# Optimization experiments

Hardware: AMD Instinct MI355X
Metric: run time of the kernel (lower is better)

Reference implementation:

```python
import jax, jax.numpy as jnp
import numpy as np

N_NODES = 100000
N_EDGES = 1600000
N_QUERY = 200000
NODE_IN = 32
EDGE_IN = 8
H = 64
L = 3
LN_EPS = 1e-5
BN_EPS = 1e-5


def setup_inputs() -> dict:
    key = jax.random.key(0)
    ks = jax.random.split(key, 24)
    s = 1.0 / np.sqrt(H)
    inp = {
        "x": jax.random.normal(ks[0], (N_NODES, NODE_IN), jnp.float32),
        "edge_index": jax.random.randint(ks[1], (2, N_EDGES), 0, N_NODES, jnp.int32),
        "edge_attr": jax.random.normal(ks[2], (N_QUERY, EDGE_IN), jnp.float32),
        "query_edge_indices": jax.random.randint(ks[3], (2, N_QUERY), 0, N_NODES, jnp.int32),
        # node encoder
        "W_enc": jax.random.normal(ks[4], (NODE_IN, H), jnp.float32) * s,
        "b_enc": jnp.zeros((H,), jnp.float32),
        # SAGE layers: lin_l acts on concat(mean, max) -> [2H, H] with bias; lin_r on root [H, H] no bias
        "Wl": jax.random.normal(ks[5], (L, 2 * H, H), jnp.float32) * s,
        "bl": jnp.zeros((L, H), jnp.float32),
        "Wr": jax.random.normal(ks[6], (L, H, H), jnp.float32) * s,
        "ln_g": jnp.ones((L, H), jnp.float32),
        "ln_b": jnp.zeros((L, H), jnp.float32),
        # edge predictor MLP
        "W1": jax.random.normal(ks[7], (2 * H + EDGE_IN, 2 * H), jnp.float32) * s,
        "b1": jnp.zeros((2 * H,), jnp.float32),
        "bn_g": jnp.ones((2 * H,), jnp.float32),
        "bn_b": jnp.zeros((2 * H,), jnp.float32),
        "bn_mean": jnp.zeros((2 * H,), jnp.float32),
        "bn_var": jnp.ones((2 * H,), jnp.float32),
        "W2": jax.random.normal(ks[8], (2 * H, H), jnp.float32) * s,
        "b2": jnp.zeros((H,), jnp.float32),
        "W3": jax.random.normal(ks[9], (H, 1), jnp.float32) * s,
        "b3": jnp.zeros((1,), jnp.float32),
    }
    return inp


def _layer_norm(x, g, b):
    mu = jnp.mean(x, axis=-1, keepdims=True)
    var = jnp.var(x, axis=-1, keepdims=True)
    return (x - mu) * jax.lax.rsqrt(var + LN_EPS) * g + b


def _sage_conv(h, src, dst, Wl, bl, Wr):
    # gather neighbor messages, scatter-reduce to targets (mean and max), then linear combine
    m = h[src]  # [E, H]
    deg = jax.ops.segment_sum(jnp.ones((src.shape[0],), h.dtype), dst, num_segments=N_NODES)
    summed = jax.ops.segment_sum(m, dst, num_segments=N_NODES)
    mean = summed / jnp.maximum(deg, 1.0)[:, None]
    mx = jax.ops.segment_max(m, dst, num_segments=N_NODES)
    mx = jnp.where(deg[:, None] > 0, mx, 0.0)  # PyG fills isolated nodes with 0
    aggr = jnp.concatenate([mean, mx], axis=-1)  # [N, 2H]
    return aggr @ Wl + bl + h @ Wr


def reference(x, edge_index, edge_attr, query_edge_indices,
              W_enc, b_enc, Wl, bl, Wr, ln_g, ln_b,
              W1, b1, bn_g, bn_b, bn_mean, bn_var, W2, b2, W3, b3):
    src, dst = edge_index[0], edge_index[1]
    h = x @ W_enc + b_enc
    for i in range(L):
        h_res = h
        h = _sage_conv(h, src, dst, Wl[i], bl[i], Wr[i])
        h = _layer_norm(h, ln_g[i], ln_b[i])
        h = jax.nn.gelu(h, approximate=False)
        h = h + h_res  # dropout is identity in eval
    h_src = h[query_edge_indices[0]]
    h_tgt = h[query_edge_indices[1]]
    z = jnp.concatenate([h_src, h_tgt, edge_attr], axis=1)  # [Q, 2H+E]
    z = z @ W1 + b1
    z = (z - bn_mean) * jax.lax.rsqrt(bn_var + BN_EPS) * bn_g + bn_b  # BN eval mode
    z = jax.nn.gelu(z, approximate=False)
    z = jax.nn.gelu(z @ W2 + b2, approximate=False)
    return z @ W3 + b3
```

## Files before the change

### kernel.cpp

```cpp
#include <hip/hip_runtime.h>
#include <math.h>

#define N_NODES 100000
#define N_EDGES 1600000
#define N_QUERY 200000
#define NODE_IN 32
#define EDGE_IN 8
#define H 64
#define LAYERS 3
#define LN_EPS 1e-5f
#define BN_EPS 1e-5f
#define NBLK 391
#define NBUK 391
#define ACHUNK 4096
#define CAPB 6144

typedef __attribute__((ext_vector_type(8))) short short8b;
typedef __attribute__((ext_vector_type(4))) float f32x4;

__device__ __forceinline__ float gelu_f(float x){
    return 0.5f * x * (1.0f + erff(x * 0.70710678118654752440f));
}
__device__ __forceinline__ ushort f2bf(float x){
    unsigned u = __float_as_uint(x);
    unsigned r = (u + 0x7FFFu + ((u >> 16) & 1u)) >> 16;
    return (ushort)r;
}
__device__ __forceinline__ float bf2f(ushort x){
    return __uint_as_float(((unsigned)x) << 16);
}

__global__ __launch_bounds__(256) void k_zero_cnt(int* __restrict__ c){
    int i = blockIdx.x * 256 + threadIdx.x;
    if (i < N_NODES) c[i] = 0;
}
__global__ __launch_bounds__(256) void k_count(const int* __restrict__ ei, int* __restrict__ c){
    int i = blockIdx.x * 256 + threadIdx.x;
    if (i < N_EDGES) atomicAdd(&c[ei[N_EDGES + i]], 1);
}
__global__ __launch_bounds__(256) void k_scanA(const int* __restrict__ cnt, int* __restrict__ bsum){
    int i = blockIdx.x * 256 + threadIdx.x;
    int v = (i < N_NODES) ? cnt[i] : 0;
    #pragma unroll
    for (int off = 32; off; off >>= 1) v += __shfl_xor(v, off, 64);
    __shared__ int ws[4];
    if ((threadIdx.x & 63) == 0) ws[threadIdx.x >> 6] = v;
    __syncthreads();
    if (threadIdx.x == 0) bsum[blockIdx.x] = ws[0] + ws[1] + ws[2] + ws[3];
}
__global__ __launch_bounds__(512) void k_scanB(int* __restrict__ bsum){
    __shared__ int s[512];
    int t = threadIdx.x;
    int v = (t < NBLK) ? bsum[t] : 0;
    s[t] = v; __syncthreads();
    for (int off = 1; off < 512; off <<= 1){
        int u = (t >= off) ? s[t - off] : 0;
        __syncthreads();
        s[t] += u;
        __syncthreads();
    }
    if (t < NBLK) bsum[t] = s[t] - v;
}
__global__ __launch_bounds__(256) void k_scanC(const int* __restrict__ cnt, const int* __restrict__ bsum,
                                               int* __restrict__ rs){
    __shared__ int s[256];
    int t = threadIdx.x;
    int i = blockIdx.x * 256 + t;
    int v = (i < N_NODES) ? cnt[i] : 0;
    s[t] = v; __syncthreads();
    for (int off = 1; off < 256; off <<= 1){
        int u = (t >= off) ? s[t - off] : 0;
        __syncthreads();
        s[t] += u;
        __syncthreads();
    }
    int pref = bsum[blockIdx.x] + s[t] - v;
    if (i < N_NODES) rs[i] = pref;
    if (i == N_NODES - 1) rs[N_NODES] = pref + v;
}
__global__ __launch_bounds__(256) void k_init_bcur(const int* __restrict__ rs, int* __restrict__ bcur){
    int b = blockIdx.x * 256 + threadIdx.x;
    if (b < NBUK) bcur[b] = rs[b * 256];
}
__global__ __launch_bounds__(1024) void k_bucketA(const int* __restrict__ ei, int* __restrict__ bcur,
                                                  int* __restrict__ bucketed){
    __shared__ int hist[NBUK], pref[NBUK], curl[NBUK], gbase[NBUK];
    __shared__ int scan[512];
    __shared__ int stageP[ACHUNK];
    __shared__ ushort stageB[ACHUNK];
    int tid = threadIdx.x;
    int e0 = blockIdx.x * ACHUNK;
    int cnt = N_EDGES - e0;
    if (cnt > ACHUNK) cnt = ACHUNK;
    for (int b = tid; b < NBUK; b += 1024) hist[b] = 0;
    __syncthreads();
    int myd[4], mys[4];
    #pragma unroll
    for (int i = 0; i < 4; ++i){
        int idx = tid + i * 1024;
        if (idx < cnt){
            int e = e0 + idx;
            mys[i] = ei[e];
            myd[i] = ei[N_EDGES + e];
            atomicAdd(&hist[myd[i] >> 8], 1);
        } else myd[i] = -1;
    }
    __syncthreads();
    int v = (tid < NBUK) ? hist[tid] : 0;
    if (tid < 512) scan[tid] = v;
    __syncthreads();
    for (int off = 1; off < 512; off <<= 1){
        int u = 0;
        if (tid < 512 && tid >= off) u = scan[tid - off];
        __syncthreads();
        if (tid < 512) scan[tid] += u;
        __syncthreads();
    }
    if (tid < NBUK){
        int ex = scan[tid] - v;
        pref[tid] = ex;
        curl[tid] = ex;
        if (v > 0) gbase[tid] = atomicAdd(&bcur[tid], v);
    }
    __syncthreads();
    #pragma unroll
    for (int i = 0; i < 4; ++i){
        if (myd[i] >= 0){
            int b = myd[i] >> 8;
            int p = atomicAdd(&curl[b], 1);
            stageP[p] = (mys[i] << 8) | (myd[i] & 255);
            stageB[p] = (ushort)b;
        }
    }
    __syncthreads();
    for (int p = tid; p < cnt; p += 1024){
        int b = stageB[p];
        bucketed[gbase[b] + (p - pref[b])] = stageP[p];
    }
}
__global__ __launch_bounds__(1024) void k_fillB(const int* __restrict__ rs, int* __restrict__ csr){
    __shared__ int packed[CAPB];
    __shared__ int sorted[CAPB];
    __shared__ int hist[256], cur[256];
    __shared__ int scan[256];
    int tid = threadIdx.x;
    int node0 = blockIdx.x * 256;
    int node1 = node0 + 256; if (node1 > N_NODES) node1 = N_NODES;
    int r0 = rs[node0], r1 = rs[node1];
    int L = r1 - r0;
    if (tid < 256) hist[tid] = 0;
    __syncthreads();
    for (int i = tid; i < L; i += 1024){
        int pk = csr[r0 + i];
        packed[i] = pk;
        atomicAdd(&hist[pk & 255], 1);
    }
    __syncthreads();
    int v = (tid < 256) ? hist[tid] : 0;
    if (tid < 256) scan[tid] = v;
    __syncthreads();
    for (int off = 1; off < 256; off <<= 1){
        int u = 0;
        if (tid < 256 && tid >= off) u = scan[tid - off];
        __syncthreads();
        if (tid < 256) scan[tid] += u;
        __syncthreads();
    }
    if (tid < 256) cur[tid] = scan[tid] - v;
    __syncthreads();
    for (int i = tid; i < L; i += 1024){
        int pk = packed[i];
        int p = atomicAdd(&cur[pk & 255], 1);
        sorted[p] = pk >> 8;
    }
    __syncthreads();
    for (int i = tid; i < L; i += 1024) csr[r0 + i] = sorted[i];
}

__global__ __launch_bounds__(256) void k_enc(const float* __restrict__ x, const float* __restrict__ Wenc,
                                             const float* __restrict__ benc, float* __restrict__ h,
                                             ushort* __restrict__ hbf){
    __shared__ __align__(16) float sW[NODE_IN * H];
    __shared__ float sx[4][NODE_IN];
    int tid = threadIdx.x;
    int lane = tid & 63;
    int w = tid >> 6;
    int n = blockIdx.x * 4 + w;
    for (int i = tid; i < NODE_IN * H; i += 256) sW[i] = Wenc[i];
    if (n < N_NODES && lane < NODE_IN) sx[w][lane] = x[n * NODE_IN + lane];
    __syncthreads();
    if (n < N_NODES){
        float acc = benc[lane];
        #pragma unroll
        for (int k = 0; k < NODE_IN; ++k)
            acc = fmaf(sx[w][k], sW[k * H + lane], acc);
        h[n * H + lane] = acc;
        hbf[n * H + lane] = f2bf(acc);
    }
}

#define NT 32
__global__ __launch_bounds__(512, 4) void k_sage_mfma(const float* __restrict__ h,
    const ushort* __restrict__ hbf,
    const int* __restrict__ rs, const int* __restrict__ csr,
    const float* __restrict__ Wl, const float* __restrict__ bl, const float* __restrict__ Wr,
    const float* __restrict__ lng, const float* __restrict__ lnb,
    float* __restrict__ hout, ushort* __restrict__ hbfout)
{
    __shared__ __align__(16) ushort sAh[NT * 200];
    __shared__ __align__(16) ushort sAl[NT * 200];
    __shared__ __align__(16) ushort sW[64 * 200];
    __shared__ float2 sRed[8][16];
    const int tid = threadIdx.x;
    const int lane = tid & 63;
    const int w = tid >> 6;
    const int l15 = lane & 15;
    const int kb = lane >> 4;
    const int c4 = l15 * 4;
    const int n0 = blockIdx.x * NT;

    for (int i = tid; i < 128 * 64; i += 512){
        int k = i >> 6, f = i & 63;
        sW[f * 200 + k] = f2bf(Wl[i]);
    }
    for (int i = tid; i < 64 * 64; i += 512){
        int k = (i >> 6) + 128, f = i & 63;
        sW[f * 200 + k] = f2bf(Wr[i]);
    }

    for (int i = 0; i < 4; ++i){
        int nl = (w << 2) + i;
        int n = n0 + nl;
        float s0 = 0.f, s1 = 0.f, s2 = 0.f, s3 = 0.f;
        float m0 = -INFINITY, m1 = -INFINITY, m2 = -INFINITY, m3 = -INFINITY;
        int dg = 0;
        float4 hv4 = make_float4(0.f, 0.f, 0.f, 0.f);
        if (n < N_NODES){
            int start = rs[n], end = rs[n + 1];
            dg = end - start;
            hv4 = *(const float4*)(h + (size_t)n * H + c4);
            const int* cp = csr + start;
            int nfull = dg >> 2;
            #pragma unroll 4
            for (int j = 0; j < nfull; ++j){
                int s = cp[j * 4 + kb];
                const ushort4 u = *(const ushort4*)(hbf + ((size_t)s << 6) + c4);
                float v0 = bf2f(u.x), v1 = bf2f(u.y), v2 = bf2f(u.z), v3 = bf2f(u.w);
                s0 += v0; s1 += v1; s2 += v2; s3 += v3;
                m0 = fmaxf(m0, v0); m1 = fmaxf(m1, v1);
                m2 = fmaxf(m2, v2); m3 = fmaxf(m3, v3);
            }
            int rem = dg & 3;
            if (rem){
                int e = nfull * 4 + kb;
                int s = cp[(kb < rem) ? e : 0];
                const ushort4 u = *(const ushort4*)(hbf + ((size_t)s << 6) + c4);
                float v0 = bf2f(u.x), v1 = bf2f(u.y), v2 = bf2f(u.z), v3 = bf2f(u.w);
                bool val = kb < rem;
                s0 += val ? v0 : 0.f;  s1 += val ? v1 : 0.f;
                s2 += val ? v2 : 0.f;  s3 += val ? v3 : 0.f;
                m0 = fmaxf(m0, val ? v0 : -INFINITY);
                m1 = fmaxf(m1, val ? v1 : -INFINITY);
                m2 = fmaxf(m2, val ? v2 : -INFINITY);
                m3 = fmaxf(m3, val ? v3 : -INFINITY);
            }
        }
        #pragma unroll
        for (int off = 16; off < 64; off <<= 1){
            s0 += __shfl_xor(s0, off, 64); s1 += __shfl_xor(s1, off, 64);
            s2 += __shfl_xor(s2, off, 64); s3 += __shfl_xor(s3, off, 64);
            m0 = fmaxf(m0, __shfl_xor(m0, off, 64)); m1 = fmaxf(m1, __shfl_xor(m1, off, 64));
            m2 = fmaxf(m2, __shfl_xor(m2, off, 64)); m3 = fmaxf(m3, __shfl_xor(m3, off, 64));
        }
        float inv = (dg > 0) ? (1.f / (float)dg) : 0.f;
        float4 val;
        if (kb == 0)      val = make_float4(s0 * inv, s1 * inv, s2 * inv, s3 * inv);
        else if (kb == 1) val = (dg > 0) ? make_float4(m0, m1, m2, m3) : make_float4(0.f,0.f,0.f,0.f);
        else              val = hv4;
        if (kb < 3){
            ushort4 vh = { f2bf(val.x), f2bf(val.y), f2bf(val.z), f2bf(val.w) };
            ushort4 vl = { f2bf(val.x - bf2f(vh.x)), f2bf(val.y - bf2f(vh.y)),
                           f2bf(val.z - bf2f(vh.z)), f2bf(val.w - bf2f(vh.w)) };
            *(ushort4*)(sAh + nl * 200 + kb * 64 + c4) = vh;
            *(ushort4*)(sAl + nl * 200 + kb * 64 + c4) = vl;
        }
    }
    __syncthreads();

    f32x4 acc = (f32x4){0.f,0.f,0.f,0.f};
    const int rt = w & 1;
    const int c0 = (w >> 1) * 16;
    const int arow = (rt * 16 + l15) * 200 + kb * 8;
    const int brow = (c0 + l15) * 200 + kb * 8;
    #pragma unroll
    for (int kc = 0; kc < 6; ++kc){
        short8b ah = *(const short8b*)(sAh + arow + kc * 32);
        short8b al = *(const short8b*)(sAl + arow + kc * 32);
        short8b b  = *(const short8b*)(sW + brow + kc * 32);
        acc = __builtin_amdgcn_mfma_f32_16x16x32_bf16(ah, b, acc, 0, 0, 0);
        acc = __builtin_amdgcn_mfma_f32_16x16x32_bf16(al, b, acc, 0, 0, 0);
    }

    const int f = c0 + l15;
    float blf = bl[f], gf = lng[f], bfv = lnb[f];
    #pragma unroll
    for (int r = 0; r < 4; ++r) acc[r] += blf;
    f32x4 s1v, s2v;
    #pragma unroll
    for (int r = 0; r < 4; ++r){ s1v[r] = acc[r]; s2v[r] = acc[r] * acc[r]; }
    #pragma unroll
    for (int r = 0; r < 4; ++r){
        #pragma unroll
        for (int off = 1; off < 16; off <<= 1){
            s1v[r] += __shfl_xor(s1v[r], off, 64);
            s2v[r] += __shfl_xor(s2v[r], off, 64);
        }
    }
    if (l15 == 0){
        #pragma unroll
        for (int r = 0; r < 4; ++r) sRed[w][kb * 4 + r] = make_float2(s1v[r], s2v[r]);
    }
    __syncthreads();
    const int rowb = n0 + rt * 16 + kb * 4;
    #pragma unroll
    for (int r = 0; r < 4; ++r){
        int row = rowb + r;
        if (row < N_NODES){
            float2 p2 = sRed[w ^ 2][kb * 4 + r];
            float2 p4 = sRed[w ^ 4][kb * 4 + r];
            float2 p6 = sRed[w ^ 6][kb * 4 + r];
            float S1 = s1v[r] + p2.x + p4.x + p6.x;
            float S2 = s2v[r] + p2.y + p4.y + p6.y;
            float mu = S1 * (1.f / 64.f);
            float var = S2 * (1.f / 64.f) - mu * mu;
            float rsv = rsqrtf(var + LN_EPS);
            float y = (acc[r] - mu) * rsv * gf + bfv;
            float o = gelu_f(y) + h[row * H + f];
            hout[row * H + f] = o;
            hbfout[row * H + f] = f2bf(o);
        }
    }
}

#define QB 128
__global__ __launch_bounds__(512, 2) void k_mlp_mfma(const ushort* __restrict__ hbf,
    const int* __restrict__ qe, const float* __restrict__ ea,
    const float* __restrict__ W1, const float* __restrict__ b1,
    const float* __restrict__ bng, const float* __restrict__ bnb,
    const float* __restrict__ bnm, const float* __restrict__ bnv,
    const float* __restrict__ W2, const float* __restrict__ b2,
    const float* __restrict__ W3, const float* __restrict__ b3,
    float* __restrict__ out)
{
    __shared__ __align__(16) ushort sZ[QB * 168];
    __shared__ __align__(16) ushort sWa[128 * 72];
    __shared__ __align__(16) ushort sWb[128 * 72];
    const int tid = threadIdx.x;
    const int lane = tid & 63;
    const int w = tid >> 6;
    const int l15 = lane & 15;
    const int kb = lane >> 4;
    const int q0 = blockIdx.x * QB;

    {
        int tq = tid >> 2;
        int part = tid & 3;
        int q = q0 + tq;
        int qs = (q < N_QUERY) ? q : 0;
        int sidx = qe[qs], tidx = qe[N_QUERY + qs];
        const ushort* srcrow = (part < 2) ? (hbf + (size_t)sidx * H + part * 32)
                                          : (hbf + (size_t)tidx * H + (part - 2) * 32);
        ushort* dst = sZ + tq * 168 + part * 32;
        *(short8b*)(dst)      = *(const short8b*)(srcrow);
        *(short8b*)(dst + 8)  = *(const short8b*)(srcrow + 8);
        *(short8b*)(dst + 16) = *(const short8b*)(srcrow + 16);
        *(short8b*)(dst + 24) = *(const short8b*)(srcrow + 24);
        if (part == 0){
            const float4* ep = (const float4*)(ea + (size_t)qs * 8);
            float4 e0 = ep[0], e1 = ep[1];
            ushort4 o0 = { f2bf(e0.x), f2bf(e0.y), f2bf(e0.z), f2bf(e0.w) };
            ushort4 o1 = { f2bf(e1.x), f2bf(e1.y), f2bf(e1.z), f2bf(e1.w) };
            *(ushort4*)(sZ + tq * 168 + 128) = o0;
            *(ushort4*)(sZ + tq * 168 + 132) = o1;
        } else {
            ushort4 zz = { 0, 0, 0, 0 };
            ushort* zp = sZ + tq * 168 + 136 + (part - 1) * 8;
            *(ushort4*)(zp) = zz;
            *(ushort4*)(zp + 4) = zz;
        }
        if (part == 3){
            ushort4 zz = { 0, 0, 0, 0 };
            *(ushort4*)(sZ + tq * 168 + 160) = zz;
            *(ushort4*)(sZ + tq * 168 + 164) = zz;
        }
    }
    for (int it = 0; it < 16; ++it){
        int idx = tid + it * 512;
        int j = idx & 127, kl = idx >> 7;
        sWa[j * 72 + kl] = f2bf(W1[(kl) * 128 + j]);
        sWb[j * 72 + kl] = f2bf(W1[(64 + kl) * 128 + j]);
    }
    __syncthreads();

    f32x4 acc[8];
    #pragma unroll
    for (int n = 0; n < 8; ++n) acc[n] = (f32x4){0.f, 0.f, 0.f, 0.f};
    const int arow = (w * 16 + l15) * 168 + kb * 8;
    #pragma unroll
    for (int s = 0; s < 4; ++s){
        const ushort* wbuf = (s < 2) ? sWa : sWb;
        int kg = s * 32;
        int kl = (s & 1) * 32;
        short8b a = *(const short8b*)(sZ + arow + kg);
        #pragma unroll
        for (int n = 0; n < 8; ++n){
            short8b b = *(const short8b*)(wbuf + (n * 16 + l15) * 72 + kl + kb * 8);
            acc[n] = __builtin_amdgcn_mfma_f32_16x16x32_bf16(a, b, acc[n], 0, 0, 0);
        }
    }
    __syncthreads();
    for (int it = 0; it < 16; ++it){
        int idx = tid + it * 512;
        int j = idx & 127, kl = idx >> 7;
        int k = 128 + kl;
        sWa[j * 72 + kl] = (k < 136) ? f2bf(W1[k * 128 + j]) : 0;
        int k2 = idx >> 6, f = idx & 63;
        sWb[f * 136 + k2] = f2bf(W2[idx]);
    }
    __syncthreads();
    {
        short8b a = *(const short8b*)(sZ + arow + 128);
        #pragma unroll
        for (int n = 0; n < 8; ++n){
            short8b b = *(const short8b*)(sWa + (n * 16 + l15) * 72 + kb * 8);
            acc[n] = __builtin_amdgcn_mfma_f32_16x16x32_bf16(a, b, acc[n], 0, 0, 0);
        }
    }
    float scn[8], shn[8];
    #pragma unroll
    for (int n = 0; n < 8; ++n){
        int j = n * 16 + l15;
        float sc = bng[j] * rsqrtf(bnv[j] + BN_EPS);
        scn[n] = sc;
        shn[n] = bnb[j] - bnm[j] * sc + b1[j] * sc;
    }
    __syncthreads();
    #pragma unroll
    for (int n = 0; n < 8; ++n){
        #pragma unroll
        for (int r = 0; r < 4; ++r){
            float v = acc[n][r] * scn[n] + shn[n];
            float g = gelu_f(v);
            sZ[(w * 16 + kb * 4 + r) * 136 + n * 16 + l15] = f2bf(g);
        }
    }
    __syncthreads();

    f32x4 acc2[4];
    #pragma unroll
    for (int n = 0; n < 4; ++n) acc2[n] = (f32x4){0.f, 0.f, 0.f, 0.f};
    const int arow2 = (w * 16 + l15) * 136 + kb * 8;
    #pragma unroll
    for (int s = 0; s < 4; ++s){
        int ks = s * 32;
        short8b a = *(const short8b*)(sZ + arow2 + ks);
        #pragma unroll
        for (int n = 0; n < 4; ++n){
            short8b b = *(const short8b*)(sWb + (n * 16 + l15) * 136 + ks + kb * 8);
            acc2[n] = __builtin_amdgcn_mfma_f32_16x16x32_bf16(a, b, acc2[n], 0, 0, 0);
        }
    }
    float b3v = b3[0];
    f32x4 pvv = (f32x4){0.f, 0.f, 0.f, 0.f};
    #pragma unroll
    for (int n = 0; n < 4; ++n){
        int f = n * 16 + l15;
        float b2f = b2[f], w3f = W3[f];
        #pragma unroll
        for (int r = 0; r < 4; ++r)
            pvv[r] += gelu_f(acc2[n][r] + b2f) * w3f;
    }
    #pragma unroll
    for (int r = 0; r < 4; ++r){
        #pragma unroll
        for (int off = 1; off < 16; off <<= 1)
            pvv[r] += __shfl_xor(pvv[r], off, 64);
    }
    if (l15 == 0){
        #pragma unroll
        for (int r = 0; r < 4; ++r){
            int q = q0 + w * 16 + kb * 4 + r;
            if (q < N_QUERY) out[q] = pvv[r] + b3v;
        }
    }
}

extern "C" void kernel_launch(void* const* d_in, const int* in_sizes, int n_in,
                              void* d_out, int out_size, void* d_ws, size_t ws_size,
                              hipStream_t stream) {
    const float* x    = (const float*)d_in[0];
    const int*   ei   = (const int*)d_in[1];
    const float* ea   = (const float*)d_in[2];
    const int*   qe   = (const int*)d_in[3];
    const float* Wenc = (const float*)d_in[4];
    const float* benc = (const float*)d_in[5];
    const float* Wl   = (const float*)d_in[6];
    const float* bl   = (const float*)d_in[7];
    const float* Wr   = (const float*)d_in[8];
    const float* lng  = (const float*)d_in[9];
    const float* lnb  = (const float*)d_in[10];
    const float* W1   = (const float*)d_in[11];
    const float* b1   = (const float*)d_in[12];
    const float* bng  = (const float*)d_in[13];
    const float* bnb  = (const float*)d_in[14];
    const float* bnm  = (const float*)d_in[15];
    const float* bnv  = (const float*)d_in[16];
    const float* W2   = (const float*)d_in[17];
    const float* b2   = (const float*)d_in[18];
    const float* W3   = (const float*)d_in[19];
    const float* b3   = (const float*)d_in[20];
    float* out = (float*)d_out;

    char* ws = (char*)d_ws;
    const size_t NH = (size_t)N_NODES * H;
    float*  hA   = (float*)ws;   ws += NH * 4;
    float*  hB   = (float*)ws;   ws += NH * 4;
    ushort* hbfA = (ushort*)ws;  ws += NH * 2;
    ushort* hbfB = (ushort*)ws;  ws += NH * 2;
    int*    cnt  = (int*)ws;     ws += (size_t)N_NODES * 4;
    int*    rsb  = (int*)ws;     ws += ((size_t)N_NODES + 4) * 4;
    int*    bcur = (int*)ws;     ws += (size_t)NBUK * 4;
    int*    csr  = (int*)ws;     ws += (size_t)N_EDGES * 4;
    int*    bsum = (int*)ws;     ws += 512 * 4;

    k_zero_cnt<<<NBLK, 256, 0, stream>>>(cnt);
    k_count<<<(N_EDGES + 255) / 256, 256, 0, stream>>>(ei, cnt);
    k_scanA<<<NBLK, 256, 0, stream>>>(cnt, bsum);
    k_scanB<<<1, 512, 0, stream>>>(bsum);
    k_scanC<<<NBLK, 256, 0, stream>>>(cnt, bsum, rsb);
    k_init_bcur<<<(NBUK + 255) / 256, 256, 0, stream>>>(rsb, bcur);
    k_bucketA<<<(N_EDGES + ACHUNK - 1) / ACHUNK, 1024, 0, stream>>>(ei, bcur, csr);
    k_fillB<<<NBUK, 1024, 0, stream>>>(rsb, csr);

    k_enc<<<(N_NODES + 3) / 4, 256, 0, stream>>>(x, Wenc, benc, hA, hbfA);

    int nbn = (N_NODES + NT - 1) / NT;
    float* hc = hA;  float* hn = hB;
    ushort* hbc = hbfA; ushort* hbn = hbfB;
    for (int l = 0; l < LAYERS; ++l){
        k_sage_mfma<<<nbn, 512, 0, stream>>>(hc, hbc, rsb, csr,
            Wl + (size_t)l * 2 * H * H, bl + l * H, Wr + (size_t)l * H * H,
            lng + l * H, lnb + l * H, hn, hbn);
        float* t1 = hc; hc = hn; hn = t1;
        ushort* t2 = hbc; hbc = hbn; hbn = t2;
    }

    int nbq = (N_QUERY + QB - 1) / QB;
    k_mlp_mfma<<<nbq, 512, 0, stream>>>(hbc, qe, ea, W1, b1, bng, bnb, bnm, bnv, W2, b2, W3, b3, out);
}
```

Before: 500.6 us.

## Split SAGE aggregation into per-feature-plane gather kernels feeding a separate GEMM

Stores the bf16 node features as four planes of 16 features each, and adds a gather kernel that aggregates mean and max for one plane at a time. Each pass then works on a small, cache-resident slice of the table instead of random full 128-byte rows. The results go to an fp32 aggr buffer, which a separate MFMA GEMM+LayerNorm kernel reads; that kernel also updates h in place and writes both planar and flat bf16 copies. The aim is better cache locality for the random neighbor gather. The cost is extra launches and a large aggr round trip through memory on every layer.

```diff
diff --git a/kernel.cpp b/kernel.cpp
--- a/kernel.cpp
+++ b/kernel.cpp
@@ -179,7 +179,7 @@
 
 __global__ __launch_bounds__(256) void k_enc(const float* __restrict__ x, const float* __restrict__ Wenc,
                                              const float* __restrict__ benc, float* __restrict__ h,
-                                             ushort* __restrict__ hbf){
+                                             ushort* __restrict__ hbfP){
     __shared__ __align__(16) float sW[NODE_IN * H];
     __shared__ float sx[4][NODE_IN];
     int tid = threadIdx.x;
@@ -195,17 +195,65 @@
         for (int k = 0; k < NODE_IN; ++k)
             acc = fmaf(sx[w][k], sW[k * H + lane], acc);
         h[n * H + lane] = acc;
-        hbf[n * H + lane] = f2bf(acc);
+        hbfP[(lane >> 4) * (N_NODES * 16) + n * 16 + (lane & 15)] = f2bf(acc);
+    }
+}
+
+#define GBLK 2048
+__global__ __launch_bounds__(256) void k_gather(const ushort* __restrict__ hbfP,
+    const int* __restrict__ rs, const int* __restrict__ csr,
+    float* __restrict__ aggr, int p)
+{
+    const int tid = threadIdx.x;
+    const int lane = tid & 63;
+    const int w = tid >> 6;
+    const int eslot = lane >> 2;
+    const int c = lane & 3;
+    const ushort* plane = hbfP + (size_t)p * (N_NODES * 16);
+    int gw = blockIdx.x * 4 + w;
+    const int nwaves = GBLK * 4;
+    for (int n = gw; n < N_NODES; n += nwaves){
+        int start = rs[n], end = rs[n + 1];
+        int dg = end - start;
+        float s0 = 0.f, s1 = 0.f, s2 = 0.f, s3 = 0.f;
+        float m0 = -INFINITY, m1 = -INFINITY, m2 = -INFINITY, m3 = -INFINITY;
+        for (int base = start; base < end; base += 16){
+            int cnt = end - base; if (cnt > 16) cnt = 16;
+            int es = (eslot < cnt) ? eslot : (cnt - 1);
+            int s = csr[base + es];
+            const ushort4 u = *(const ushort4*)(plane + (size_t)s * 16 + c * 4);
+            float v0 = bf2f(u.x), v1 = bf2f(u.y), v2 = bf2f(u.z), v3 = bf2f(u.w);
+            bool val = eslot < cnt;
+            s0 += val ? v0 : 0.f;  s1 += val ? v1 : 0.f;
+            s2 += val ? v2 : 0.f;  s3 += val ? v3 : 0.f;
+            m0 = fmaxf(m0, val ? v0 : -INFINITY);
+            m1 = fmaxf(m1, val ? v1 : -INFINITY);
+            m2 = fmaxf(m2, val ? v2 : -INFINITY);
+            m3 = fmaxf(m3, val ? v3 : -INFINITY);
+        }
+        #pragma unroll
+        for (int off = 4; off < 64; off <<= 1){
+            s0 += __shfl_xor(s0, off, 64); s1 += __shfl_xor(s1, off, 64);
+            s2 += __shfl_xor(s2, off, 64); s3 += __shfl_xor(s3, off, 64);
+            m0 = fmaxf(m0, __shfl_xor(m0, off, 64)); m1 = fmaxf(m1, __shfl_xor(m1, off, 64));
+            m2 = fmaxf(m2, __shfl_xor(m2, off, 64)); m3 = fmaxf(m3, __shfl_xor(m3, off, 64));
+        }
+        if (lane < 4){
+            float inv = (dg > 0) ? (1.f / (float)dg) : 0.f;
+            float4 mean = make_float4(s0 * inv, s1 * inv, s2 * inv, s3 * inv);
+            float4 mx = (dg > 0) ? make_float4(m0, m1, m2, m3) : make_float4(0.f, 0.f, 0.f, 0.f);
+            *(float4*)(aggr + (size_t)n * 128 + p * 16 + lane * 4) = mean;
+            *(float4*)(aggr + (size_t)n * 128 + 64 + p * 16 + lane * 4) = mx;
+        }
     }
 }
 
 #define NT 32
-__global__ __launch_bounds__(512, 4) void k_sage_mfma(const float* __restrict__ h,
-    const ushort* __restrict__ hbf,
-    const int* __restrict__ rs, const int* __restrict__ csr,
+__global__ __launch_bounds__(512, 4) void k_sage_gemm(float* __restrict__ h,
+    const float* __restrict__ aggr,
     const float* __restrict__ Wl, const float* __restrict__ bl, const float* __restrict__ Wr,
     const float* __restrict__ lng, const float* __restrict__ lnb,
-    float* __restrict__ hout, ushort* __restrict__ hbfout)
+    ushort* __restrict__ hbfP, ushort* __restrict__ hbfFlat)
 {
     __shared__ __align__(16) ushort sAh[NT * 200];
     __shared__ __align__(16) ushort sAl[NT * 200];
@@ -216,7 +264,6 @@
     const int w = tid >> 6;
     const int l15 = lane & 15;
     const int kb = lane >> 4;
-    const int c4 = l15 * 4;
     const int n0 = blockIdx.x * NT;
 
     for (int i = tid; i < 128 * 64; i += 512){
@@ -227,62 +274,23 @@
         int k = (i >> 6) + 128, f = i & 63;
         sW[f * 200 + k] = f2bf(Wr[i]);
     }
-
     for (int i = 0; i < 4; ++i){
         int nl = (w << 2) + i;
         int n = n0 + nl;
-        float s0 = 0.f, s1 = 0.f, s2 = 0.f, s3 = 0.f;
-        float m0 = -INFINITY, m1 = -INFINITY, m2 = -INFINITY, m3 = -INFINITY;
-        int dg = 0;
-        float4 hv4 = make_float4(0.f, 0.f, 0.f, 0.f);
         if (n < N_NODES){
-            int start = rs[n], end = rs[n + 1];
-            dg = end - start;
-            hv4 = *(const float4*)(h + (size_t)n * H + c4);
-            const int* cp = csr + start;
-            int nfull = dg >> 2;
-            #pragma unroll 4
-            for (int j = 0; j < nfull; ++j){
-                int s = cp[j * 4 + kb];
-                const ushort4 u = *(const ushort4*)(hbf + ((size_t)s << 6) + c4);
-                float v0 = bf2f(u.x), v1 = bf2f(u.y), v2 = bf2f(u.z), v3 = bf2f(u.w);
-                s0 += v0; s1 += v1; s2 += v2; s3 += v3;
-                m0 = fmaxf(m0, v0); m1 = fmaxf(m1, v1);
-                m2 = fmaxf(m2, v2); m3 = fmaxf(m3, v3);
-            }
-            int rem = dg & 3;
-            if (rem){
-                int e = nfull * 4 + kb;
-                int s = cp[(kb < rem) ? e : 0];
-                const ushort4 u = *(const ushort4*)(hbf + ((size_t)s << 6) + c4);
-                float v0 = bf2f(u.x), v1 = bf2f(u.y), v2 = bf2f(u.z), v3 = bf2f(u.w);
-                bool val = kb < rem;
-                s0 += val ? v0 : 0.f;  s1 += val ? v1 : 0.f;
-                s2 += val ? v2 : 0.f;  s3 += val ? v3 : 0.f;
-                m0 = fmaxf(m0, val ? v0 : -INFINITY);
-                m1 = fmaxf(m1, val ? v1 : -INFINITY);
-                m2 = fmaxf(m2, val ? v2 : -INFINITY);
-                m3 = fmaxf(m3, val ? v3 : -INFINITY);
-            }
-        }
-        #pragma unroll
-        for (int off = 16; off < 64; off <<= 1){
-            s0 += __shfl_xor(s0, off, 64); s1 += __shfl_xor(s1, off, 64);
-            s2 += __shfl_xor(s2, off, 64); s3 += __shfl_xor(s3, off, 64);
-            m0 = fmaxf(m0, __shfl_xor(m0, off, 64)); m1 = fmaxf(m1, __shfl_xor(m1, off, 64));
-            m2 = fmaxf(m2, __shfl_xor(m2, off, 64)); m3 = fmaxf(m3, __shfl_xor(m3, off, 64));
-        }
-        float inv = (dg > 0) ? (1.f / (float)dg) : 0.f;
-        float4 val;
-        if (kb == 0)      val = make_float4(s0 * inv, s1 * inv, s2 * inv, s3 * inv);
-        else if (kb == 1) val = (dg > 0) ? make_float4(m0, m1, m2, m3) : make_float4(0.f,0.f,0.f,0.f);
-        else              val = hv4;
-        if (kb < 3){
-            ushort4 vh = { f2bf(val.x), f2bf(val.y), f2bf(val.z), f2bf(val.w) };
-            ushort4 vl = { f2bf(val.x - bf2f(vh.x)), f2bf(val.y - bf2f(vh.y)),
-                           f2bf(val.z - bf2f(vh.z)), f2bf(val.w - bf2f(vh.w)) };
-            *(ushort4*)(sAh + nl * 200 + kb * 64 + c4) = vh;
-            *(ushort4*)(sAl + nl * 200 + kb * 64 + c4) = vl;
+            float2 a = *(const float2*)(aggr + (size_t)n * 128 + lane * 2);
+            ushort hx = f2bf(a.x), hy = f2bf(a.y);
+            *(ushort2*)(sAh + nl * 200 + lane * 2) = (ushort2){ hx, hy };
+            *(ushort2*)(sAl + nl * 200 + lane * 2) = (ushort2){ f2bf(a.x - bf2f(hx)), f2bf(a.y - bf2f(hy)) };
+            float hv = h[(size_t)n * H + lane];
+            ushort hh = f2bf(hv);
+            sAh[nl * 200 + 128 + lane] = hh;
+            sAl[nl * 200 + 128 + lane] = f2bf(hv - bf2f(hh));
+        } else {
+            *(ushort2*)(sAh + nl * 200 + lane * 2) = (ushort2){ 0, 0 };
+            *(ushort2*)(sAl + nl * 200 + lane * 2) = (ushort2){ 0, 0 };
+            sAh[nl * 200 + 128 + lane] = 0;
+            sAl[nl * 200 + 128 + lane] = 0;
         }
     }
     __syncthreads();
@@ -335,9 +343,11 @@
             float var = S2 * (1.f / 64.f) - mu * mu;
             float rsv = rsqrtf(var + LN_EPS);
             float y = (acc[r] - mu) * rsv * gf + bfv;
-            float o = gelu_f(y) + h[row * H + f];
-            hout[row * H + f] = o;
-            hbfout[row * H + f] = f2bf(o);
+            float o = gelu_f(y) + h[(size_t)row * H + f];
+            ushort ob = f2bf(o);
+            h[(size_t)row * H + f] = o;
+            hbfP[(w >> 1) * (N_NODES * 16) + row * 16 + l15] = ob;
+            hbfFlat[(size_t)row * H + f] = ob;
         }
     }
 }
@@ -523,15 +533,15 @@
 
     char* ws = (char*)d_ws;
     const size_t NH = (size_t)N_NODES * H;
-    float*  hA   = (float*)ws;   ws += NH * 4;
-    float*  hB   = (float*)ws;   ws += NH * 4;
-    ushort* hbfA = (ushort*)ws;  ws += NH * 2;
-    ushort* hbfB = (ushort*)ws;  ws += NH * 2;
-    int*    cnt  = (int*)ws;     ws += (size_t)N_NODES * 4;
-    int*    rsb  = (int*)ws;     ws += ((size_t)N_NODES + 4) * 4;
-    int*    bcur = (int*)ws;     ws += (size_t)NBUK * 4;
-    int*    csr  = (int*)ws;     ws += (size_t)N_EDGES * 4;
-    int*    bsum = (int*)ws;     ws += 512 * 4;
+    float*  h     = (float*)ws;   ws += NH * 4;
+    ushort* hbfP  = (ushort*)ws;  ws += NH * 2;
+    ushort* hbfF  = (ushort*)ws;  ws += NH * 2;
+    float*  aggr  = (float*)ws;   ws += (size_t)N_NODES * 128 * 4;
+    int*    cnt   = (int*)ws;     ws += (size_t)N_NODES * 4;
+    int*    rsb   = (int*)ws;     ws += ((size_t)N_NODES + 4) * 4;
+    int*    bcur  = (int*)ws;     ws += (size_t)NBUK * 4;
+    int*    csr   = (int*)ws;     ws += (size_t)N_EDGES * 4;
+    int*    bsum  = (int*)ws;     ws += 512 * 4;
 
     k_zero_cnt<<<NBLK, 256, 0, stream>>>(cnt);
     k_count<<<(N_EDGES + 255) / 256, 256, 0, stream>>>(ei, cnt);
@@ -542,19 +552,17 @@
     k_bucketA<<<(N_EDGES + ACHUNK - 1) / ACHUNK, 1024, 0, stream>>>(ei, bcur, csr);
     k_fillB<<<NBUK, 1024, 0, stream>>>(rsb, csr);
 
-    k_enc<<<(N_NODES + 3) / 4, 256, 0, stream>>>(x, Wenc, benc, hA, hbfA);
+    k_enc<<<(N_NODES + 3) / 4, 256, 0, stream>>>(x, Wenc, benc, h, hbfP);
 
     int nbn = (N_NODES + NT - 1) / NT;
-    float* hc = hA;  float* hn = hB;
-    ushort* hbc = hbfA; ushort* hbn = hbfB;
     for (int l = 0; l < LAYERS; ++l){
-        k_sage_mfma<<<nbn, 512, 0, stream>>>(hc, hbc, rsb, csr,
+        for (int p = 0; p < 4; ++p)
+            k_gather<<<GBLK, 256, 0, stream>>>(hbfP, rsb, csr, aggr, p);
+        k_sage_gemm<<<nbn, 512, 0, stream>>>(h, aggr,
             Wl + (size_t)l * 2 * H * H, bl + l * H, Wr + (size_t)l * H * H,
-            lng + l * H, lnb + l * H, hn, hbn);
-        float* t1 = hc; hc = hn; hn = t1;
-        ushort* t2 = hbc; hbc = hbn; hbn = t2;
+            lng + l * H, lnb + l * H, hbfP, hbfF);
     }
 
     int nbq = (N_QUERY + QB - 1) / QB;
-    k_mlp_mfma<<<nbq, 512, 0, stream>>>(hbc, qe, ea, W1, b1, bng, bnb, bnm, bnv, W2, b2, W3, b3, out);
-}
+    k_mlp_mfma<<<nbq, 512, 0, stream>>>(hbfF, qe, ea, W1, b1, bng, bnb, bnm, bnv, W2, b2, W3, b3, out);
+}
```

Measured after the change: 869.7 us. 1.74x slower.

## Make edge MLP kernel persistent with weights staged once per block

Applied to the files above, without the earlier changes.

Replaces the one-tile-per-block MLP kernel with a persistent grid of 512 blocks that converts W1 and W2 to bf16 in shared memory once and then loops over 64-query tiles. Waves now split the output columns in halves, and partial results from the two halves are combined through shared memory. The goal is to avoid reloading and converting the weights for every 128-query tile. In exchange there are more barriers per tile and fewer rows per wave, which may lower MFMA utilisation and latency hiding. The code also assumes N_QUERY divides evenly by 64 and drops the bounds checks.

```diff
diff --git a/kernel.cpp b/kernel.cpp
--- a/kernel.cpp
+++ b/kernel.cpp
@@ -342,8 +342,10 @@
     }
 }
 
-#define QB 128
-__global__ __launch_bounds__(512, 2) void k_mlp_mfma(const ushort* __restrict__ hbf,
+#define QB2 64
+#define MLP_TILES (N_QUERY / QB2)
+#define MLP_GRID 512
+__global__ __launch_bounds__(512, 2) void k_mlp2(const ushort* __restrict__ hbf,
     const int* __restrict__ qe, const float* __restrict__ ea,
     const float* __restrict__ W1, const float* __restrict__ b1,
     const float* __restrict__ bng, const float* __restrict__ bnb,
@@ -352,146 +354,140 @@
     const float* __restrict__ W3, const float* __restrict__ b3,
     float* __restrict__ out)
 {
-    __shared__ __align__(16) ushort sZ[QB * 168];
-    __shared__ __align__(16) ushort sWa[128 * 72];
-    __shared__ __align__(16) ushort sWb[128 * 72];
+    __shared__ __align__(16) ushort sW1[128 * 136 + 32];
+    __shared__ __align__(16) ushort sW2[64 * 136];
+    __shared__ __align__(16) ushort sZ[QB2 * 168];
+    __shared__ float sRedO[8][16];
     const int tid = threadIdx.x;
     const int lane = tid & 63;
     const int w = tid >> 6;
     const int l15 = lane & 15;
     const int kb = lane >> 4;
-    const int q0 = blockIdx.x * QB;
-
-    {
-        int tq = tid >> 2;
-        int part = tid & 3;
-        int q = q0 + tq;
-        int qs = (q < N_QUERY) ? q : 0;
-        int sidx = qe[qs], tidx = qe[N_QUERY + qs];
-        const ushort* srcrow = (part < 2) ? (hbf + (size_t)sidx * H + part * 32)
-                                          : (hbf + (size_t)tidx * H + (part - 2) * 32);
-        ushort* dst = sZ + tq * 168 + part * 32;
-        *(short8b*)(dst)      = *(const short8b*)(srcrow);
-        *(short8b*)(dst + 8)  = *(const short8b*)(srcrow + 8);
-        *(short8b*)(dst + 16) = *(const short8b*)(srcrow + 16);
-        *(short8b*)(dst + 24) = *(const short8b*)(srcrow + 24);
-        if (part == 0){
-            const float4* ep = (const float4*)(ea + (size_t)qs * 8);
-            float4 e0 = ep[0], e1 = ep[1];
-            ushort4 o0 = { f2bf(e0.x), f2bf(e0.y), f2bf(e0.z), f2bf(e0.w) };
-            ushort4 o1 = { f2bf(e1.x), f2bf(e1.y), f2bf(e1.z), f2bf(e1.w) };
-            *(ushort4*)(sZ + tq * 168 + 128) = o0;
-            *(ushort4*)(sZ + tq * 168 + 132) = o1;
-        } else {
-            ushort4 zz = { 0, 0, 0, 0 };
-            ushort* zp = sZ + tq * 168 + 136 + (part - 1) * 8;
-            *(ushort4*)(zp) = zz;
-            *(ushort4*)(zp + 4) = zz;
-        }
-        if (part == 3){
-            ushort4 zz = { 0, 0, 0, 0 };
-            *(ushort4*)(sZ + tq * 168 + 160) = zz;
-            *(ushort4*)(sZ + tq * 168 + 164) = zz;
-        }
-    }
-    for (int it = 0; it < 16; ++it){
-        int idx = tid + it * 512;
-        int j = idx & 127, kl = idx >> 7;
-        sWa[j * 72 + kl] = f2bf(W1[(kl) * 128 + j]);
-        sWb[j * 72 + kl] = f2bf(W1[(64 + kl) * 128 + j]);
-    }
-    __syncthreads();
-
-    f32x4 acc[8];
-    #pragma unroll
-    for (int n = 0; n < 8; ++n) acc[n] = (f32x4){0.f, 0.f, 0.f, 0.f};
-    const int arow = (w * 16 + l15) * 168 + kb * 8;
-    #pragma unroll
-    for (int s = 0; s < 4; ++s){
-        const ushort* wbuf = (s < 2) ? sWa : sWb;
-        int kg = s * 32;
-        int kl = (s & 1) * 32;
-        short8b a = *(const short8b*)(sZ + arow + kg);
-        #pragma unroll
-        for (int n = 0; n < 8; ++n){
-            short8b b = *(const short8b*)(wbuf + (n * 16 + l15) * 72 + kl + kb * 8);
-            acc[n] = __builtin_amdgcn_mfma_f32_16x16x32_bf16(a, b, acc[n], 0, 0, 0);
-        }
-    }
-    __syncthreads();
-    for (int it = 0; it < 16; ++it){
-        int idx = tid + it * 512;
-        int j = idx & 127, kl = idx >> 7;
-        int k = 128 + kl;
-        sWa[j * 72 + kl] = (k < 136) ? f2bf(W1[k * 128 + j]) : 0;
-        int k2 = idx >> 6, f = idx & 63;
-        sWb[f * 136 + k2] = f2bf(W2[idx]);
-    }
-    __syncthreads();
-    {
-        short8b a = *(const short8b*)(sZ + arow + 128);
-        #pragma unroll
-        for (int n = 0; n < 8; ++n){
-            short8b b = *(const short8b*)(sWa + (n * 16 + l15) * 72 + kb * 8);
-            acc[n] = __builtin_amdgcn_mfma_f32_16x16x32_bf16(a, b, acc[n], 0, 0, 0);
-        }
-    }
-    float scn[8], shn[8];
-    #pragma unroll
-    for (int n = 0; n < 8; ++n){
-        int j = n * 16 + l15;
+    const int rt = w & 3;
+    const int whalf = w >> 2;
+
+    for (int i = tid; i < 136 * 128; i += 512){
+        int k = i >> 7, j = i & 127;
+        sW1[j * 136 + k] = f2bf(W1[i]);
+    }
+    if (tid < 32) sW1[128 * 136 + tid] = 0;
+    for (int i = tid; i < 64 * 128; i += 512){
+        int k = i >> 6, f = i & 63;
+        sW2[f * 136 + k] = f2bf(W2[i]);
+    }
+    float scn[4], shn[4];
+    #pragma unroll
+    for (int n = 0; n < 4; ++n){
+        int j = whalf * 64 + n * 16 + l15;
         float sc = bng[j] * rsqrtf(bnv[j] + BN_EPS);
         scn[n] = sc;
         shn[n] = bnb[j] - bnm[j] * sc + b1[j] * sc;
     }
-    __syncthreads();
-    #pragma unroll
-    for (int n = 0; n < 8; ++n){
+    float b2f[2], w3f[2];
+    #pragma unroll
+    for (int n = 0; n < 2; ++n){
+        int f = whalf * 32 + n * 16 + l15;
+        b2f[n] = b2[f]; w3f[n] = W3[f];
+    }
+    float b3v = b3[0];
+    __syncthreads();
+
+    for (int t = blockIdx.x; t < MLP_TILES; t += MLP_GRID){
+        int q0 = t * QB2;
+        {
+            int tq = tid >> 3, part = tid & 7;
+            int q = q0 + tq;
+            ushort* dst = sZ + tq * 168;
+            if (part < 4){
+                int sidx = qe[q];
+                const ushort* src = hbf + (size_t)sidx * H + part * 16;
+                *(short8b*)(dst + part * 16)     = *(const short8b*)(src);
+                *(short8b*)(dst + part * 16 + 8) = *(const short8b*)(src + 8);
+            } else {
+                int tidx = qe[N_QUERY + q];
+                const ushort* src = hbf + (size_t)tidx * H + (part - 4) * 16;
+                *(short8b*)(dst + 64 + (part - 4) * 16)     = *(const short8b*)(src);
+                *(short8b*)(dst + 64 + (part - 4) * 16 + 8) = *(const short8b*)(src + 8);
+                ushort4 zz = { 0, 0, 0, 0 };
+                *(ushort4*)(dst + 136 + (part - 4) * 8)     = zz;
+                *(ushort4*)(dst + 136 + (part - 4) * 8 + 4) = zz;
+            }
+            if (part == 0){
+                const float4* ep = (const float4*)(ea + (size_t)q * 8);
+                float4 e0 = ep[0], e1 = ep[1];
+                ushort4 o0 = { f2bf(e0.x), f2bf(e0.y), f2bf(e0.z), f2bf(e0.w) };
+                ushort4 o1 = { f2bf(e1.x), f2bf(e1.y), f2bf(e1.z), f2bf(e1.w) };
+                *(ushort4*)(dst + 128) = o0;
+                *(ushort4*)(dst + 132) = o1;
+            }
+        }
+        __syncthreads();
+
+        f32x4 acc[4];
+        #pragma unroll
+        for (int n = 0; n < 4; ++n) acc[n] = (f32x4){0.f, 0.f, 0.f, 0.f};
+        const int arow = (rt * 16 + l15) * 168 + kb * 8;
+        #pragma unroll
+        for (int kc = 0; kc < 5; ++kc){
+            short8b a = *(const short8b*)(sZ + arow + kc * 32);
+            #pragma unroll
+            for (int n = 0; n < 4; ++n){
+                int j = whalf * 64 + n * 16 + l15;
+                short8b b = *(const short8b*)(sW1 + j * 136 + kc * 32 + kb * 8);
+                acc[n] = __builtin_amdgcn_mfma_f32_16x16x32_bf16(a, b, acc[n], 0, 0, 0);
+            }
+        }
+        __syncthreads();
+        #pragma unroll
+        for (int n = 0; n < 4; ++n){
+            #pragma unroll
+            for (int r = 0; r < 4; ++r){
+                float v = acc[n][r] * scn[n] + shn[n];
+                sZ[(rt * 16 + kb * 4 + r) * 136 + whalf * 64 + n * 16 + l15] = f2bf(gelu_f(v));
+            }
+        }
+        __syncthreads();
+
+        f32x4 acc2[2];
+        acc2[0] = (f32x4){0.f,0.f,0.f,0.f};
+        acc2[1] = (f32x4){0.f,0.f,0.f,0.f};
+        const int arow2 = (rt * 16 + l15) * 136 + kb * 8;
+        #pragma unroll
+        for (int s = 0; s < 4; ++s){
+            short8b a = *(const short8b*)(sZ + arow2 + s * 32);
+            #pragma unroll
+            for (int n = 0; n < 2; ++n){
+                int f = whalf * 32 + n * 16 + l15;
+                short8b b = *(const short8b*)(sW2 + f * 136 + s * 32 + kb * 8);
+                acc2[n] = __builtin_amdgcn_mfma_f32_16x16x32_bf16(a, b, acc2[n], 0, 0, 0);
+            }
+        }
+        f32x4 pv = (f32x4){0.f,0.f,0.f,0.f};
+        #pragma unroll
+        for (int n = 0; n < 2; ++n){
+            #pragma unroll
+            for (int r = 0; r < 4; ++r)
+                pv[r] += gelu_f(acc2[n][r] + b2f[n]) * w3f[n];
+        }
         #pragma unroll
         for (int r = 0; r < 4; ++r){
-            float v = acc[n][r] * scn[n] + shn[n];
-            float g = gelu_f(v);
-            sZ[(w * 16 + kb * 4 + r) * 136 + n * 16 + l15] = f2bf(g);
-        }
-    }
-    __syncthreads();
-
-    f32x4 acc2[4];
-    #pragma unroll
-    for (int n = 0; n < 4; ++n) acc2[n] = (f32x4){0.f, 0.f, 0.f, 0.f};
-    const int arow2 = (w * 16 + l15) * 136 + kb * 8;
-    #pragma unroll
-    for (int s = 0; s < 4; ++s){
-        int ks = s * 32;
-        short8b a = *(const short8b*)(sZ + arow2 + ks);
-        #pragma unroll
-        for (int n = 0; n < 4; ++n){
-            short8b b = *(const short8b*)(sWb + (n * 16 + l15) * 136 + ks + kb * 8);
-            acc2[n] = __builtin_amdgcn_mfma_f32_16x16x32_bf16(a, b, acc2[n], 0, 0, 0);
-        }
-    }
-    float b3v = b3[0];
-    f32x4 pvv = (f32x4){0.f, 0.f, 0.f, 0.f};
-    #pragma unroll
-    for (int n = 0; n < 4; ++n){
-        int f = n * 16 + l15;
-        float b2f = b2[f], w3f = W3[f];
-        #pragma unroll
-        for (int r = 0; r < 4; ++r)
-            pvv[r] += gelu_f(acc2[n][r] + b2f) * w3f;
-    }
-    #pragma unroll
-    for (int r = 0; r < 4; ++r){
-        #pragma unroll
-        for (int off = 1; off < 16; off <<= 1)
-            pvv[r] += __shfl_xor(pvv[r], off, 64);
-    }
-    if (l15 == 0){
-        #pragma unroll
-        for (int r = 0; r < 4; ++r){
-            int q = q0 + w * 16 + kb * 4 + r;
-            if (q < N_QUERY) out[q] = pvv[r] + b3v;
-        }
+            #pragma unroll
+            for (int off = 1; off < 16; off <<= 1)
+                pv[r] += __shfl_xor(pv[r], off, 64);
+        }
+        if (l15 == 0){
+            #pragma unroll
+            for (int r = 0; r < 4; ++r) sRedO[w][kb * 4 + r] = pv[r];
+        }
+        __syncthreads();
+        if (whalf == 0 && l15 == 0){
+            #pragma unroll
+            for (int r = 0; r < 4; ++r){
+                int q = q0 + rt * 16 + kb * 4 + r;
+                out[q] = pv[r] + sRedO[w ^ 4][kb * 4 + r] + b3v;
+            }
+        }
+        __syncthreads();
     }
 }
 
@@ -555,6 +551,5 @@
         ushort* t2 = hbc; hbc = hbn; hbn = t2;
     }
 
-    int nbq = (N_QUERY + QB - 1) / QB;
-    k_mlp_mfma<<<nbq, 512, 0, stream>>>(hbc, qe, ea, W1, b1, bng, bnb, bnm, bnv, W2, b2, W3, b3, out);
-}
+    k_mlp2<<<MLP_GRID, 512, 0, stream>>>(hbc, qe, ea, W1, b1, bng, bnb, bnm, bnv, W2, b2, W3, b3, out);
+}
```

Result: faster. 482.2 us (-3.7%).
